# Kernel optimization log

Measured on AMD Instinct MI355X. Metric: run time of the kernel, lower is better.

The kernel has to match this reference:

```python
import jax, jax.numpy as jnp
import numpy as np


def setup_inputs() -> dict:
    key = jax.random.key(0)
    k1, k2 = jax.random.split(key)
    lut = jax.random.normal(k1, (1, 3, 33, 33, 33), dtype=jnp.float32)
    x = jax.random.uniform(k2, (8, 3, 1024, 1024), dtype=jnp.float32)
    return {"lut": lut, "x": x}


def reference(lut, x):
    # lut: [1, 3, D, D, D]; x: [B, 3, H, W] in [0,1]
    D = lut.shape[-1]
    lut0 = lut[0]  # [3, D, D, D], broadcast over batch (lut batch == 1)

    v = jnp.clip(x, 0.0, 1.0) * (D - 1)            # [B, 3, H, W]
    v = jnp.transpose(v, (0, 2, 3, 1))             # [B, H, W, 3]
    i0 = jnp.floor(v).astype(jnp.int32)            # [B, H, W, 3]
    i1 = jnp.minimum(i0 + 1, D - 1)
    f = v - i0.astype(v.dtype)                     # fractional part

    r0, g0, b0 = i0[..., 0], i0[..., 1], i0[..., 2]
    r1, g1, b1 = i1[..., 0], i1[..., 1], i1[..., 2]
    fr, fg, fb = f[..., 0], f[..., 1], f[..., 2]

    def gather(rr, gg, bb):
        # lut0[:, rr, gg, bb] -> [3, B, H, W] -> [B, 3, H, W]
        return jnp.transpose(lut0[:, rr, gg, bb], (1, 0, 2, 3))

    c000 = gather(r0, g0, b0)
    c100 = gather(r1, g0, b0)
    c010 = gather(r0, g1, b0)
    c110 = gather(r1, g1, b0)
    c001 = gather(r0, g0, b1)
    c101 = gather(r1, g0, b1)
    c011 = gather(r0, g1, b1)
    c111 = gather(r1, g1, b1)

    one = jnp.float32(1.0)
    w000 = ((one - fr) * (one - fg) * (one - fb))[:, None]
    w100 = (fr * (one - fg) * (one - fb))[:, None]
    w010 = ((one - fr) * fg * (one - fb))[:, None]
    w110 = (fr * fg * (one - fb))[:, None]
    w001 = ((one - fr) * (one - fg) * fb)[:, None]
    w101 = (fr * (one - fg) * fb)[:, None]
    w011 = ((one - fr) * fg * fb)[:, None]
    w111 = (fr * fg * fb)[:, None]

    out = (c000 * w000 + c100 * w100 + c010 * w010 + c110 * w110 +
           c001 * w001 + c101 * w101 + c011 * w011 + c111 * w111)
    return out  # [B, 3, H, W]
```

## Files before the change

### kernel.cpp

```cpp
#include <hip/hip_runtime.h>


#define D   33
#define D2  (33 * 33)
#define D3  (33 * 33 * 33)
#define HW  (1024 * 1024)
#define BATCH 8
#define QHW (HW / 4)
#define NG  (BATCH * QHW)
#define CHUNKS 256
#define GPC (NG / CHUNKS)
#define THREADS 1024

__global__ __launch_bounds__(THREADS) void lut3d_kernel(
    const float* __restrict__ lut, const float* __restrict__ x,
    float* __restrict__ out)
{
    const int c     = blockIdx.x;
    const int chunk = blockIdx.y;

    __shared__ float ls[D3];
    {
        const float* lc = lut + c * D3;
        for (int i = threadIdx.x; i < D3; i += THREADS) ls[i] = lc[i];
    }
    __syncthreads();

    const int tid  = threadIdx.x;
    const int base = chunk * GPC;

    #pragma unroll 1
    for (int it = 0; it < GPC / THREADS; ++it) {
        const int g = base + it * THREADS + tid;
        const int b = g >> 18;
        const int p = (g & (QHW - 1)) * 4;

        const float* xb = x + (size_t)b * 3 * HW + p;
        const float4 xr = *(const float4*)(xb);
        const float4 xg = *(const float4*)(xb + HW);
        const float4 xB = *(const float4*)(xb + 2 * HW);

        const float rr[4] = {xr.x, xr.y, xr.z, xr.w};
        const float gg[4] = {xg.x, xg.y, xg.z, xg.w};
        const float bb[4] = {xB.x, xB.y, xB.z, xB.w};
        float oo[4];

        #pragma unroll
        for (int j = 0; j < 4; ++j) {
            const float vr = fminf(fmaxf(rr[j], 0.f), 1.f) * 32.f;
            const float vg = fminf(fmaxf(gg[j], 0.f), 1.f) * 32.f;
            const float vb = fminf(fmaxf(bb[j], 0.f), 1.f) * 32.f;

            const float r0f = floorf(vr);
            const float g0f = floorf(vg);
            const float b0f = floorf(vb);
            const int r0 = (int)r0f, g0 = (int)g0f, b0 = (int)b0f;
            const float fr = vr - r0f, fg = vg - g0f, fb = vb - b0f;

            const int dr = (r0 < D - 1) ? D2 : 0;
            const int dg = (g0 < D - 1) ? D  : 0;
            const int db = (b0 < D - 1) ? 1  : 0;
            const int idx = r0 * D2 + g0 * D + b0;

            const float c000 = ls[idx];
            const float c001 = ls[idx + db];
            const float c010 = ls[idx + dg];
            const float c011 = ls[idx + dg + db];
            const float c100 = ls[idx + dr];
            const float c101 = ls[idx + dr + db];
            const float c110 = ls[idx + dr + dg];
            const float c111 = ls[idx + dr + dg + db];

            const float c00 = c000 + fb * (c001 - c000);
            const float c01 = c010 + fb * (c011 - c010);
            const float c10 = c100 + fb * (c101 - c100);
            const float c11 = c110 + fb * (c111 - c110);
            const float c0  = c00 + fg * (c01 - c00);
            const float c1  = c10 + fg * (c11 - c10);
            oo[j] = c0 + fr * (c1 - c0);
        }

        float* ob = out + (size_t)b * 3 * HW + (size_t)c * HW + p;
        *(float4*)ob = make_float4(oo[0], oo[1], oo[2], oo[3]);
    }
}

extern "C" void kernel_launch(void* const* d_in, const int* in_sizes, int n_in,
                              void* d_out, int out_size, void* d_ws, size_t ws_size,
                              hipStream_t stream) {
    const float* lut = (const float*)d_in[0];
    const float* x   = (const float*)d_in[1];
    float* out = (float*)d_out;

    dim3 grid(3, CHUNKS);
    lut3d_kernel<<<grid, THREADS, 0, stream>>>(lut, x, out);
}
```

Before: 211.5 us.

## Pack LUT neighbor pairs as half2 in LDS and remap blocks per XCD

The LUT is stored in shared memory as half2 pairs of adjacent b-entries, so each sample needs four LDS reads instead of eight. Clamping the scaled value just below 32 lets the code drop the edge-case offset logic. The block index is remapped so the three channel blocks of each chunk land on the same XCD, aiming to share the input reads in L2. In exchange the LUT values are rounded to fp16, which lowers accuracy and may exceed the tolerance.

```diff
diff --git a/kernel.cpp b/kernel.cpp
--- a/kernel.cpp
+++ b/kernel.cpp
@@ -1,9 +1,11 @@
 #include <hip/hip_runtime.h>
+#include <hip/hip_fp16.h>
 
 
 #define D   33
 #define D2  (33 * 33)
 #define D3  (33 * 33 * 33)
+#define NP  (D3 - 1)
 #define HW  (1024 * 1024)
 #define BATCH 8
 #define QHW (HW / 4)
@@ -11,18 +13,27 @@
 #define CHUNKS 256
 #define GPC (NG / CHUNKS)
 #define THREADS 1024
+#define NXCD 8
+#define CPX (CHUNKS / NXCD)
 
 __global__ __launch_bounds__(THREADS) void lut3d_kernel(
     const float* __restrict__ lut, const float* __restrict__ x,
     float* __restrict__ out)
 {
-    const int c     = blockIdx.x;
-    const int chunk = blockIdx.y;
+    const int bid = blockIdx.x;
+    const int xcd = bid & (NXCD - 1);
+    const int s   = bid >> 3;
+    const int cl  = s / 3;
+    const int c   = s - 3 * cl;
+    const int chunk = xcd * CPX + cl;
 
-    __shared__ float ls[D3];
+    __shared__ __half2 ls[NP];
     {
         const float* lc = lut + c * D3;
-        for (int i = threadIdx.x; i < D3; i += THREADS) ls[i] = lc[i];
+        for (int i = threadIdx.x; i < NP; i += THREADS) {
+            ls[i] = __halves2half2(__float2half_rn(lc[i]),
+                                   __float2half_rn(lc[i + 1]));
+        }
     }
     __syncthreads();
 
@@ -47,36 +58,30 @@
 
         #pragma unroll
         for (int j = 0; j < 4; ++j) {
-            const float vr = fminf(fmaxf(rr[j], 0.f), 1.f) * 32.f;
-            const float vg = fminf(fmaxf(gg[j], 0.f), 1.f) * 32.f;
-            const float vb = fminf(fmaxf(bb[j], 0.f), 1.f) * 32.f;
+            const float vr = fminf(fmaxf(rr[j], 0.f) * 32.f, 31.999998f);
+            const float vg = fminf(fmaxf(gg[j], 0.f) * 32.f, 31.999998f);
+            const float vb = fminf(fmaxf(bb[j], 0.f) * 32.f, 31.999998f);
 
-            const float r0f = floorf(vr);
-            const float g0f = floorf(vg);
-            const float b0f = floorf(vb);
-            const int r0 = (int)r0f, g0 = (int)g0f, b0 = (int)b0f;
-            const float fr = vr - r0f, fg = vg - g0f, fb = vb - b0f;
+            const int r0 = (int)vr, g0 = (int)vg, b0 = (int)vb;
+            const float fr = vr - (float)r0;
+            const float fg = vg - (float)g0;
+            const float fb = vb - (float)b0;
 
-            const int dr = (r0 < D - 1) ? D2 : 0;
-            const int dg = (g0 < D - 1) ? D  : 0;
-            const int db = (b0 < D - 1) ? 1  : 0;
-            const int idx = r0 * D2 + g0 * D + b0;
+            const int idx = __mul24(r0, D2) + __mul24(g0, D) + b0;
 
-            const float c000 = ls[idx];
-            const float c001 = ls[idx + db];
-            const float c010 = ls[idx + dg];
-            const float c011 = ls[idx + dg + db];
-            const float c100 = ls[idx + dr];
-            const float c101 = ls[idx + dr + db];
-            const float c110 = ls[idx + dr + dg];
-            const float c111 = ls[idx + dr + dg + db];
+            const __half2 h00 = ls[idx];
+            const __half2 h01 = ls[idx + D];
+            const __half2 h10 = ls[idx + D2];
+            const __half2 h11 = ls[idx + D2 + D];
 
-            const float c00 = c000 + fb * (c001 - c000);
-            const float c01 = c010 + fb * (c011 - c010);
-            const float c10 = c100 + fb * (c101 - c100);
-            const float c11 = c110 + fb * (c111 - c110);
-            const float c0  = c00 + fg * (c01 - c00);
-            const float c1  = c10 + fg * (c11 - c10);
+            const float wb0 = 1.0f - fb;
+            const float c00 = __low2float(h00) * wb0 + __high2float(h00) * fb;
+            const float c01 = __low2float(h01) * wb0 + __high2float(h01) * fb;
+            const float c10 = __low2float(h10) * wb0 + __high2float(h10) * fb;
+            const float c11 = __low2float(h11) * wb0 + __high2float(h11) * fb;
+
+            const float c0 = c00 + fg * (c01 - c00);
+            const float c1 = c10 + fg * (c11 - c10);
             oo[j] = c0 + fr * (c1 - c0);
         }
 
@@ -92,6 +97,6 @@
     const float* x   = (const float*)d_in[1];
     float* out = (float*)d_out;
 
-    dim3 grid(3, CHUNKS);
+    dim3 grid(3 * CHUNKS);
     lut3d_kernel<<<grid, THREADS, 0, stream>>>(lut, x, out);
 }
```

Result: slower. 221.5 us (+4.8%).
